# Kernel tuning notes

Hardware: AMD Instinct MI355X
Metric: run time of the kernel (lower is better)

Reference implementation:

```python
import jax, jax.numpy as jnp
import numpy as np

B, N, C, H, W = 4, 5, 64, 96, 288
DOWNSAMPLE_RATE = 4
DISCRETE_RATIO = 0.4
DECAY_WEIGHTS = jax.nn.softmax(jnp.array([1.0, 0.5], dtype=jnp.float32))  # frame=1, decay=0.5


def _warp_one(img, theta):
    # img: (C,H,W), theta: (2,3). Matches F.affine_grid + F.grid_sample
    # (bilinear, zeros padding, align_corners=True).
    c, h, w = img.shape
    xs = jnp.linspace(-1.0, 1.0, w, dtype=img.dtype)
    ys = jnp.linspace(-1.0, 1.0, h, dtype=img.dtype)
    gy, gx = jnp.meshgrid(ys, xs, indexing='ij')
    base = jnp.stack([gx.ravel(), gy.ravel(), jnp.ones(h * w, img.dtype)], 0)  # (3, HW)
    g = theta @ base  # (2, HW) normalized coords
    px = (g[0] + 1.0) * 0.5 * (w - 1)
    py = (g[1] + 1.0) * 0.5 * (h - 1)
    x0 = jnp.floor(px); y0 = jnp.floor(py)
    wx = px - x0; wy = py - y0
    def tap(yy, xx):
        yi = jnp.clip(yy, 0, h - 1).astype(jnp.int32)
        xi = jnp.clip(xx, 0, w - 1).astype(jnp.int32)
        valid = ((yy >= 0) & (yy <= h - 1) & (xx >= 0) & (xx <= w - 1)).astype(img.dtype)
        return img[:, yi, xi] * valid  # (C, HW)
    out = (tap(y0, x0) * (1 - wx) * (1 - wy)
           + tap(y0, x0 + 1) * wx * (1 - wy)
           + tap(y0 + 1, x0) * (1 - wx) * wy
           + tap(y0 + 1, x0 + 1) * wx * wy)
    return out.reshape(c, h, w)


def _frame_score(hist, mlp_w, mlp_b):
    # hist: (B,N,C,H,W) -> per-pixel ego-vs-neighbor attention score (B,N,1,H,W).
    b, n, c, h, w = hist.shape
    node = hist.reshape(b, n, c, h * w).transpose(0, 3, 1, 2)  # (B, P, N, C)
    ego = node[:, :, 0]          # (B, P, C)
    neigh = node[:, :, 1:]       # (B, P, N-1, C)
    # Query rows are all the repeated ego vector -> one row suffices (identical math).
    s = jnp.einsum('bpc,bpkc->bpk', ego, neigh) / jnp.sqrt(jnp.asarray(c, hist.dtype))
    attn = jax.nn.softmax(s, axis=-1)
    ctx = jnp.einsum('bpk,bpkc->bpc', attn, neigh)
    sc = jax.nn.sigmoid(ctx @ mlp_w.T + mlp_b)                   # (B, P, 1)
    sc = jnp.broadcast_to(sc[:, :, None, :], (b, h * w, n - 1, 1))
    ego_sc = jnp.ones((b, h * w, 1, 1), hist.dtype)
    overall = jnp.concatenate([ego_sc, sc], axis=2)              # (B, P, N, 1)
    return overall.transpose(0, 2, 3, 1).reshape(b, n, 1, h, w)


def _forward(x0, x1, pairwise_t_matrix, mlp_w, mlp_b):
    x0g = x0.reshape(B, N, C, H, W)
    x1g = x1.reshape(B, N, C, H, W)

    # --- TemporalSampling: weighted per-frame scores, threshold, 3x3 max-pool ---
    conf = DECAY_WEIGHTS[0] * _frame_score(x0g, mlp_w, mlp_b) \
         + DECAY_WEIGHTS[1] * _frame_score(x1g, mlp_w, mlp_b)      # (B,N,1,H,W)
    mask = jnp.where(conf > 0.5, jnp.float32(1.0), jnp.float32(0.0))
    mask = jax.lax.reduce_window(mask, -jnp.inf, jax.lax.max,
                                 (1, 1, 1, 3, 3), (1, 1, 1, 1, 1), 'SAME')
    x = x0g * mask  # broadcast over C

    # --- normalize pairwise transform to 2x3 affine matrices ---
    t = pairwise_t_matrix[:, :, :, jnp.array([0, 1])][:, :, :, :, jnp.array([0, 1, 3])]  # (B,L,L,2,3)
    t = t.at[..., 0, 1].mul(H / W)
    t = t.at[..., 1, 0].mul(W / H)
    t = t.at[..., 0, 2].set(t[..., 0, 2] / (DOWNSAMPLE_RATE * DISCRETE_RATIO * W) * 2)
    t = t.at[..., 1, 2].set(t[..., 1, 2] / (DOWNSAMPLE_RATE * DISCRETE_RATIO * H) * 2)
    theta = t[:, 0]  # (B,N,2,3): warp each cav into ego frame

    # --- per-agent warp ---
    warped = jax.vmap(jax.vmap(_warp_one))(x, theta)  # (B,N,C,H,W)

    # --- AttenFusion: per-pixel NxN attention, keep ego row ---
    nf = warped.reshape(B, N, C, H * W).transpose(0, 3, 1, 2)  # (B, P, N, C)
    s = jnp.einsum('bpc,bpkc->bpk', nf[:, :, 0], nf) / jnp.sqrt(jnp.asarray(C, nf.dtype))
    attn = jax.nn.softmax(s, axis=-1)
    ctx = jnp.einsum('bpk,bpkc->bpc', attn, nf)                 # (B, P, C)
    x_fuse = ctx.transpose(0, 2, 1).reshape(B, C, H, W)
    return x_fuse


def setup_inputs() -> dict:
    key = jax.random.key(0)
    k0, k1, k2, k3 = jax.random.split(key, 4)
    x0 = jax.random.normal(k0, (B * N, C, H, W), dtype=jnp.float32)
    x1 = jax.random.normal(k1, (B * N, C, H, W), dtype=jnp.float32)
    eye = jnp.broadcast_to(jnp.eye(4, dtype=jnp.float32), (B, N, N, 4, 4))
    pairwise_t_matrix = eye + 0.01 * jax.random.normal(k2, (B, N, N, 4, 4), dtype=jnp.float32)
    mlp_w = 0.1 * jax.random.normal(k3, (1, C), dtype=jnp.float32)
    mlp_b = jnp.zeros((1,), dtype=jnp.float32)
    record_len = jnp.full((B,), N, dtype=jnp.int32)
    return {"x0": x0, "x1": x1, "pairwise_t_matrix": pairwise_t_matrix,
            "mlp_w": mlp_w, "mlp_b": mlp_b, "record_len": record_len}


def reference(x0, x1, pairwise_t_matrix, mlp_w, mlp_b, record_len):
    # record_len is uniform (=N) and only determines the static regrouping.
    return _forward(x0, x1, pairwise_t_matrix, mlp_w, mlp_b)
```

## Files before the change

### kernel.cpp

```cpp
#include <hip/hip_runtime.h>
#include <cmath>

#define BB 4
#define NN 5
#define CC 64
#define HH 96
#define WW 288
#define PP (HH*WW)

static __device__ __forceinline__ float sigmoidf_(float x) {
    return 1.0f / (1.0f + expf(-x));
}

__global__ __launch_bounds__(256) void mask_kernel(
    const float* __restrict__ x0, const float* __restrict__ x1,
    const float* __restrict__ mlp_w, const float* __restrict__ mlp_b,
    float* __restrict__ premask)
{
    int idx = blockIdx.x * blockDim.x + threadIdx.x;
    if (idx >= BB * PP) return;
    int b = idx / PP;
    int p = idx - b * PP;
    float bias = mlp_b[0];

    float scv[2];
    const float* bases[2];
    bases[0] = x0 + (size_t)b * NN * CC * PP + p;
    bases[1] = x1 + (size_t)b * NN * CC * PP + p;

    #pragma unroll
    for (int t = 0; t < 2; t++) {
        const float* base = bases[t];
        float dot0 = 0.f, dot1 = 0.f, dot2 = 0.f, dot3 = 0.f;
        float mw0 = 0.f, mw1 = 0.f, mw2 = 0.f, mw3 = 0.f;
        for (int c = 0; c < CC; c++) {
            const float* q = base + (size_t)c * PP;
            float e  = q[0];
            float wc = mlp_w[c];
            float v1 = q[(size_t)1 * CC * PP];
            float v2 = q[(size_t)2 * CC * PP];
            float v3 = q[(size_t)3 * CC * PP];
            float v4 = q[(size_t)4 * CC * PP];
            dot0 += e * v1;  mw0 += wc * v1;
            dot1 += e * v2;  mw1 += wc * v2;
            dot2 += e * v3;  mw2 += wc * v3;
            dot3 += e * v4;  mw3 += wc * v4;
        }
        float s0 = dot0 * 0.125f, s1 = dot1 * 0.125f;
        float s2 = dot2 * 0.125f, s3 = dot3 * 0.125f;
        float m = fmaxf(fmaxf(s0, s1), fmaxf(s2, s3));
        float e0 = expf(s0 - m), e1 = expf(s1 - m);
        float e2 = expf(s2 - m), e3 = expf(s3 - m);
        float inv = 1.0f / (e0 + e1 + e2 + e3);
        float z = (e0 * mw0 + e1 * mw1 + e2 * mw2 + e3 * mw3) * inv + bias;
        scv[t] = sigmoidf_(z);
    }
    const float W0 = 0.6224593312018546f, W1 = 0.3775406687981454f;
    float conf = W0 * scv[0] + W1 * scv[1];
    premask[idx] = (conf > 0.5f) ? 1.0f : 0.0f;
}

__global__ __launch_bounds__(256) void pool_kernel(
    const float* __restrict__ pre, float* __restrict__ pooled)
{
    int idx = blockIdx.x * blockDim.x + threadIdx.x;
    if (idx >= BB * PP) return;
    int b = idx / PP;
    int p = idx - b * PP;
    int h = p / WW;
    int w = p - h * WW;
    const float* pb = pre + (size_t)b * PP;
    float m = 0.0f;
    #pragma unroll
    for (int dy = -1; dy <= 1; dy++) {
        int y = h + dy;
        if (y < 0 || y >= HH) continue;
        #pragma unroll
        for (int dx = -1; dx <= 1; dx++) {
            int x = w + dx;
            if (x < 0 || x >= WW) continue;
            m = fmaxf(m, pb[y * WW + x]);
        }
    }
    pooled[idx] = m;
}

__global__ __launch_bounds__(256) void fuse_kernel(
    const float* __restrict__ x0, const float* __restrict__ pmat,
    const float* __restrict__ pooled, float* __restrict__ out)
{
    int idx = blockIdx.x * blockDim.x + threadIdx.x;
    if (idx >= BB * PP) return;
    int b = idx / PP;
    int p = idx - b * PP;
    int h = p / WW;
    int w = p - h * WW;

    float gx = -1.0f + 2.0f * (float)w / (float)(WW - 1);
    float gy = -1.0f + 2.0f * (float)h / (float)(HH - 1);

    int   offs[NN][4];
    float wts[NN][4];

    #pragma unroll
    for (int n = 0; n < NN; n++) {
        const float* m = pmat + ((size_t)(b * NN + 0) * NN + n) * 16;
        float t00 = m[0];
        float t01 = m[1] * ((float)HH / (float)WW);
        float t02 = m[3] * (float)(2.0 / (4.0 * 0.4 * (double)WW));
        float t10 = m[4] * ((float)WW / (float)HH);
        float t11 = m[5];
        float t12 = m[7] * (float)(2.0 / (4.0 * 0.4 * (double)HH));

        float g0 = t00 * gx + t01 * gy + t02;
        float g1 = t10 * gx + t11 * gy + t12;
        float px = (g0 + 1.0f) * 0.5f * (float)(WW - 1);
        float py = (g1 + 1.0f) * 0.5f * (float)(HH - 1);
        float x0f = floorf(px), y0f = floorf(py);
        float wx = px - x0f, wy = py - y0f;

        float bw[4] = { (1.f - wx) * (1.f - wy), wx * (1.f - wy),
                        (1.f - wx) * wy,         wx * wy };
        #pragma unroll
        for (int t = 0; t < 4; t++) {
            float xx = (t & 1) ? (x0f + 1.0f) : x0f;
            float yy = (t >> 1) ? (y0f + 1.0f) : y0f;
            int xi = min(max((int)xx, 0), WW - 1);
            int yi = min(max((int)yy, 0), HH - 1);
            float valid = (yy >= 0.0f && yy <= (float)(HH - 1) &&
                           xx >= 0.0f && xx <= (float)(WW - 1)) ? 1.0f : 0.0f;
            float mk = (n == 0) ? 1.0f : pooled[b * PP + yi * WW + xi];
            offs[n][t] = yi * WW + xi;
            wts[n][t]  = bw[t] * valid * mk;
        }
    }

    const float* base = x0 + (size_t)b * NN * CC * PP;

    float dot[NN] = {0.f, 0.f, 0.f, 0.f, 0.f};
    for (int c = 0; c < CC; c++) {
        float v[NN];
        #pragma unroll
        for (int n = 0; n < NN; n++) {
            const float* pl = base + ((size_t)n * CC + c) * PP;
            float acc = 0.f;
            #pragma unroll
            for (int t = 0; t < 4; t++)
                acc += wts[n][t] * pl[offs[n][t]];
            v[n] = acc;
        }
        #pragma unroll
        for (int n = 0; n < NN; n++)
            dot[n] += v[0] * v[n];
    }

    float s[NN], attn[NN];
    float mx = -INFINITY;
    #pragma unroll
    for (int n = 0; n < NN; n++) { s[n] = dot[n] * 0.125f; mx = fmaxf(mx, s[n]); }
    float sum = 0.f;
    #pragma unroll
    for (int n = 0; n < NN; n++) { attn[n] = expf(s[n] - mx); sum += attn[n]; }
    float inv = 1.0f / sum;
    #pragma unroll
    for (int n = 0; n < NN; n++) attn[n] *= inv;

    for (int c = 0; c < CC; c++) {
        float o = 0.f;
        #pragma unroll
        for (int n = 0; n < NN; n++) {
            const float* pl = base + ((size_t)n * CC + c) * PP;
            float acc = 0.f;
            #pragma unroll
            for (int t = 0; t < 4; t++)
                acc += wts[n][t] * pl[offs[n][t]];
            o += attn[n] * acc;
        }
        out[((size_t)b * CC + c) * PP + p] = o;
    }
}

extern "C" void kernel_launch(void* const* d_in, const int* in_sizes, int n_in,
                              void* d_out, int out_size, void* d_ws, size_t ws_size,
                              hipStream_t stream) {
    const float* x0    = (const float*)d_in[0];
    const float* x1    = (const float*)d_in[1];
    const float* pmat  = (const float*)d_in[2];
    const float* mlp_w = (const float*)d_in[3];
    const float* mlp_b = (const float*)d_in[4];
    float* out = (float*)d_out;

    const size_t need = (size_t)2 * BB * PP * sizeof(float);
    float* pre;
    float* pooled;
    if (ws_size >= need && d_ws != nullptr) {
        pre    = (float*)d_ws;
        pooled = pre + (size_t)BB * PP;
    } else {
        pre    = out;
        pooled = (float*)d_in[1];
    }

    int total = BB * PP;
    dim3 blk(256);
    dim3 grd((total + 255) / 256);

    mask_kernel<<<grd, blk, 0, stream>>>(x0, x1, mlp_w, mlp_b, pre);
    pool_kernel<<<grd, blk, 0, stream>>>(pre, pooled);
    fuse_kernel<<<grd, blk, 0, stream>>>(x0, pmat, pooled, out);
}
```

Measured before the change: 407.4 us.

## Split channel loops across grid dimension with partial-sum kernels

```diff
diff --git a/kernel.cpp b/kernel.cpp
--- a/kernel.cpp
+++ b/kernel.cpp
@@ -7,101 +7,21 @@
 #define HH 96
 #define WW 288
 #define PP (HH*WW)
+#define BP (BB*PP)
+#define CP (CC*PP)
+#define NCP (NN*CC*PP)
+
 
 static __device__ __forceinline__ float sigmoidf_(float x) {
     return 1.0f / (1.0f + expf(-x));
 }
 
-__global__ __launch_bounds__(256) void mask_kernel(
-    const float* __restrict__ x0, const float* __restrict__ x1,
-    const float* __restrict__ mlp_w, const float* __restrict__ mlp_b,
-    float* __restrict__ premask)
-{
-    int idx = blockIdx.x * blockDim.x + threadIdx.x;
-    if (idx >= BB * PP) return;
-    int b = idx / PP;
-    int p = idx - b * PP;
-    float bias = mlp_b[0];
-
-    float scv[2];
-    const float* bases[2];
-    bases[0] = x0 + (size_t)b * NN * CC * PP + p;
-    bases[1] = x1 + (size_t)b * NN * CC * PP + p;
-
-    #pragma unroll
-    for (int t = 0; t < 2; t++) {
-        const float* base = bases[t];
-        float dot0 = 0.f, dot1 = 0.f, dot2 = 0.f, dot3 = 0.f;
-        float mw0 = 0.f, mw1 = 0.f, mw2 = 0.f, mw3 = 0.f;
-        for (int c = 0; c < CC; c++) {
-            const float* q = base + (size_t)c * PP;
-            float e  = q[0];
-            float wc = mlp_w[c];
-            float v1 = q[(size_t)1 * CC * PP];
-            float v2 = q[(size_t)2 * CC * PP];
-            float v3 = q[(size_t)3 * CC * PP];
-            float v4 = q[(size_t)4 * CC * PP];
-            dot0 += e * v1;  mw0 += wc * v1;
-            dot1 += e * v2;  mw1 += wc * v2;
-            dot2 += e * v3;  mw2 += wc * v3;
-            dot3 += e * v4;  mw3 += wc * v4;
-        }
-        float s0 = dot0 * 0.125f, s1 = dot1 * 0.125f;
-        float s2 = dot2 * 0.125f, s3 = dot3 * 0.125f;
-        float m = fmaxf(fmaxf(s0, s1), fmaxf(s2, s3));
-        float e0 = expf(s0 - m), e1 = expf(s1 - m);
-        float e2 = expf(s2 - m), e3 = expf(s3 - m);
-        float inv = 1.0f / (e0 + e1 + e2 + e3);
-        float z = (e0 * mw0 + e1 * mw1 + e2 * mw2 + e3 * mw3) * inv + bias;
-        scv[t] = sigmoidf_(z);
-    }
-    const float W0 = 0.6224593312018546f, W1 = 0.3775406687981454f;
-    float conf = W0 * scv[0] + W1 * scv[1];
-    premask[idx] = (conf > 0.5f) ? 1.0f : 0.0f;
-}
-
-__global__ __launch_bounds__(256) void pool_kernel(
-    const float* __restrict__ pre, float* __restrict__ pooled)
-{
-    int idx = blockIdx.x * blockDim.x + threadIdx.x;
-    if (idx >= BB * PP) return;
-    int b = idx / PP;
-    int p = idx - b * PP;
-    int h = p / WW;
-    int w = p - h * WW;
-    const float* pb = pre + (size_t)b * PP;
-    float m = 0.0f;
-    #pragma unroll
-    for (int dy = -1; dy <= 1; dy++) {
-        int y = h + dy;
-        if (y < 0 || y >= HH) continue;
-        #pragma unroll
-        for (int dx = -1; dx <= 1; dx++) {
-            int x = w + dx;
-            if (x < 0 || x >= WW) continue;
-            m = fmaxf(m, pb[y * WW + x]);
-        }
-    }
-    pooled[idx] = m;
-}
-
-__global__ __launch_bounds__(256) void fuse_kernel(
-    const float* __restrict__ x0, const float* __restrict__ pmat,
-    const float* __restrict__ pooled, float* __restrict__ out)
-{
-    int idx = blockIdx.x * blockDim.x + threadIdx.x;
-    if (idx >= BB * PP) return;
-    int b = idx / PP;
-    int p = idx - b * PP;
-    int h = p / WW;
-    int w = p - h * WW;
-
+static __device__ __forceinline__ void tap_setup(
+    int b, int h, int w, const float* __restrict__ pmat,
+    const float* __restrict__ pooled, int offs[NN][4], float wts[NN][4])
+{
     float gx = -1.0f + 2.0f * (float)w / (float)(WW - 1);
     float gy = -1.0f + 2.0f * (float)h / (float)(HH - 1);
-
-    int   offs[NN][4];
-    float wts[NN][4];
-
     #pragma unroll
     for (int n = 0; n < NN; n++) {
         const float* m = pmat + ((size_t)(b * NN + 0) * NN + n) * 16;
@@ -118,7 +38,6 @@
         float py = (g1 + 1.0f) * 0.5f * (float)(HH - 1);
         float x0f = floorf(px), y0f = floorf(py);
         float wx = px - x0f, wy = py - y0f;
-
         float bw[4] = { (1.f - wx) * (1.f - wy), wx * (1.f - wy),
                         (1.f - wx) * wy,         wx * wy };
         #pragma unroll
@@ -134,11 +53,118 @@
             wts[n][t]  = bw[t] * valid * mk;
         }
     }
-
-    const float* base = x0 + (size_t)b * NN * CC * PP;
-
-    float dot[NN] = {0.f, 0.f, 0.f, 0.f, 0.f};
-    for (int c = 0; c < CC; c++) {
+}
+
+__global__ __launch_bounds__(256) void mask_part_kernel(
+    const float* __restrict__ x0, const float* __restrict__ x1,
+    const float* __restrict__ mlp_w, float* __restrict__ mpart)
+{
+    int idx = blockIdx.x * blockDim.x + threadIdx.x;
+    int seg = blockIdx.y;
+    int b = idx / PP;
+    int p = idx - b * PP;
+    const float* xt = (seg >> 2) ? x1 : x0;
+    int c0 = (seg & 3) * 16;
+    const float* base = xt + (size_t)b * NCP + p;
+
+    float d0=0.f,d1=0.f,d2=0.f,d3=0.f, m0=0.f,m1=0.f,m2=0.f,m3=0.f;
+    #pragma unroll 4
+    for (int ci = 0; ci < 16; ci++) {
+        int c = c0 + ci;
+        const float* q = base + (size_t)c * PP;
+        float e  = q[0];
+        float wc = mlp_w[c];
+        float v1 = q[(size_t)1 * CP];
+        float v2 = q[(size_t)2 * CP];
+        float v3 = q[(size_t)3 * CP];
+        float v4 = q[(size_t)4 * CP];
+        d0 += e * v1;  m0 += wc * v1;
+        d1 += e * v2;  m1 += wc * v2;
+        d2 += e * v3;  m2 += wc * v3;
+        d3 += e * v4;  m3 += wc * v4;
+    }
+    float vals[8] = {d0,d1,d2,d3,m0,m1,m2,m3};
+    #pragma unroll
+    for (int j = 0; j < 8; j++)
+        mpart[((size_t)seg * 8 + j) * BP + idx] = vals[j];
+}
+
+__global__ __launch_bounds__(256) void mask_comb_kernel(
+    const float* __restrict__ mpart, const float* __restrict__ mlp_b,
+    float* __restrict__ premask)
+{
+    int idx = blockIdx.x * blockDim.x + threadIdx.x;
+    float bias = mlp_b[0];
+    float scv[2];
+    #pragma unroll
+    for (int t = 0; t < 2; t++) {
+        float d[4] = {0.f,0.f,0.f,0.f};
+        float m[4] = {0.f,0.f,0.f,0.f};
+        #pragma unroll
+        for (int cs = 0; cs < 4; cs++) {
+            int seg = t * 4 + cs;
+            #pragma unroll
+            for (int j = 0; j < 4; j++) {
+                d[j] += mpart[((size_t)seg * 8 + j) * BP + idx];
+                m[j] += mpart[((size_t)seg * 8 + 4 + j) * BP + idx];
+            }
+        }
+        float s0 = d[0]*0.125f, s1 = d[1]*0.125f, s2 = d[2]*0.125f, s3 = d[3]*0.125f;
+        float mx = fmaxf(fmaxf(s0, s1), fmaxf(s2, s3));
+        float e0 = expf(s0-mx), e1 = expf(s1-mx), e2 = expf(s2-mx), e3 = expf(s3-mx);
+        float inv = 1.0f / (e0+e1+e2+e3);
+        float z = (e0*m[0] + e1*m[1] + e2*m[2] + e3*m[3]) * inv + bias;
+        scv[t] = sigmoidf_(z);
+    }
+    const float W0 = 0.6224593312018546f, W1 = 0.3775406687981454f;
+    float conf = W0 * scv[0] + W1 * scv[1];
+    premask[idx] = (conf > 0.5f) ? 1.0f : 0.0f;
+}
+
+__global__ __launch_bounds__(256) void pool_kernel(
+    const float* __restrict__ pre, float* __restrict__ pooled)
+{
+    int idx = blockIdx.x * blockDim.x + threadIdx.x;
+    int b = idx / PP;
+    int p = idx - b * PP;
+    int h = p / WW;
+    int w = p - h * WW;
+    const float* pb = pre + (size_t)b * PP;
+    float m = 0.0f;
+    #pragma unroll
+    for (int dy = -1; dy <= 1; dy++) {
+        int y = h + dy;
+        if (y < 0 || y >= HH) continue;
+        #pragma unroll
+        for (int dx = -1; dx <= 1; dx++) {
+            int x = w + dx;
+            if (x < 0 || x >= WW) continue;
+            m = fmaxf(m, pb[y * WW + x]);
+        }
+    }
+    pooled[idx] = m;
+}
+
+__global__ __launch_bounds__(256) void dot_part_kernel(
+    const float* __restrict__ x0, const float* __restrict__ pmat,
+    const float* __restrict__ pooled, float* __restrict__ dpart)
+{
+    int idx = blockIdx.x * blockDim.x + threadIdx.x;
+    int seg = blockIdx.y;
+    int b = idx / PP;
+    int p = idx - b * PP;
+    int h = p / WW;
+    int w = p - h * WW;
+
+    int offs[NN][4];
+    float wts[NN][4];
+    tap_setup(b, h, w, pmat, pooled, offs, wts);
+
+    const float* base = x0 + (size_t)b * NCP;
+    float dot[NN] = {0.f,0.f,0.f,0.f,0.f};
+    #pragma unroll 4
+    for (int ci = 0; ci < 16; ci++) {
+        int c = seg * 16 + ci;
         float v[NN];
         #pragma unroll
         for (int n = 0; n < NN; n++) {
@@ -153,7 +179,31 @@
         for (int n = 0; n < NN; n++)
             dot[n] += v[0] * v[n];
     }
-
+    #pragma unroll
+    for (int n = 0; n < NN; n++)
+        dpart[((size_t)n * 4 + seg) * BP + idx] = dot[n];
+}
+
+__global__ __launch_bounds__(256) void attn_kernel(
+    const float* __restrict__ dpart, const float* __restrict__ pmat,
+    const float* __restrict__ pooled, float* __restrict__ aw,
+    int* __restrict__ offout)
+{
+    int idx = blockIdx.x * blockDim.x + threadIdx.x;
+    int b = idx / PP;
+    int p = idx - b * PP;
+    int h = p / WW;
+    int w = p - h * WW;
+
+    float dot[NN];
+    #pragma unroll
+    for (int n = 0; n < NN; n++) {
+        float s = 0.f;
+        #pragma unroll
+        for (int seg = 0; seg < 4; seg++)
+            s += dpart[((size_t)n * 4 + seg) * BP + idx];
+        dot[n] = s;
+    }
     float s[NN], attn[NN];
     float mx = -INFINITY;
     #pragma unroll
@@ -162,50 +212,84 @@
     #pragma unroll
     for (int n = 0; n < NN; n++) { attn[n] = expf(s[n] - mx); sum += attn[n]; }
     float inv = 1.0f / sum;
-    #pragma unroll
-    for (int n = 0; n < NN; n++) attn[n] *= inv;
-
-    for (int c = 0; c < CC; c++) {
-        float o = 0.f;
-        #pragma unroll
-        for (int n = 0; n < NN; n++) {
-            const float* pl = base + ((size_t)n * CC + c) * PP;
-            float acc = 0.f;
-            #pragma unroll
-            for (int t = 0; t < 4; t++)
-                acc += wts[n][t] * pl[offs[n][t]];
-            o += attn[n] * acc;
-        }
-        out[((size_t)b * CC + c) * PP + p] = o;
-    }
+
+    int offs[NN][4];
+    float wts[NN][4];
+    tap_setup(b, h, w, pmat, pooled, offs, wts);
+    #pragma unroll
+    for (int n = 0; n < NN; n++) {
+        float a = attn[n] * inv;
+        #pragma unroll
+        for (int t = 0; t < 4; t++) {
+            aw[((size_t)n * 4 + t) * BP + idx]     = a * wts[n][t];
+            offout[((size_t)n * 4 + t) * BP + idx] = offs[n][t];
+        }
+    }
+}
+
+__global__ __launch_bounds__(256) void out_kernel(
+    const float* __restrict__ x0, const float* __restrict__ aw,
+    const int* __restrict__ offin, float* __restrict__ out)
+{
+    int idx = blockIdx.x * blockDim.x + threadIdx.x;
+    int c0  = blockIdx.y * 4;
+    int b = idx / PP;
+    int p = idx - b * PP;
+
+    float a[20];
+    int   o[20];
+    #pragma unroll
+    for (int j = 0; j < 20; j++) {
+        a[j] = aw[(size_t)j * BP + idx];
+        o[j] = offin[(size_t)j * BP + idx];
+    }
+
+    const float* base = x0 + (size_t)b * NCP + (size_t)c0 * PP;
+    float acc0 = 0.f, acc1 = 0.f, acc2 = 0.f, acc3 = 0.f;
+    #pragma unroll
+    for (int j = 0; j < 20; j++) {
+        int n = j >> 2;
+        const float* pl = base + (size_t)n * CP + o[j];
+        float w = a[j];
+        acc0 += w * pl[0];
+        acc1 += w * pl[(size_t)1 * PP];
+        acc2 += w * pl[(size_t)2 * PP];
+        acc3 += w * pl[(size_t)3 * PP];
+    }
+    size_t ob = ((size_t)b * CC + c0) * PP + p;
+    out[ob]                 = acc0;
+    out[ob + (size_t)1*PP]  = acc1;
+    out[ob + (size_t)2*PP]  = acc2;
+    out[ob + (size_t)3*PP]  = acc3;
 }
 
 extern "C" void kernel_launch(void* const* d_in, const int* in_sizes, int n_in,
                               void* d_out, int out_size, void* d_ws, size_t ws_size,
                               hipStream_t stream) {
     const float* x0    = (const float*)d_in[0];
-    const float* x1    = (const float*)d_in[1];
+    float*       x1    = (float*)d_in[1];
     const float* pmat  = (const float*)d_in[2];
     const float* mlp_w = (const float*)d_in[3];
     const float* mlp_b = (const float*)d_in[4];
     float* out = (float*)d_out;
 
-    const size_t need = (size_t)2 * BB * PP * sizeof(float);
-    float* pre;
-    float* pooled;
-    if (ws_size >= need && d_ws != nullptr) {
-        pre    = (float*)d_ws;
-        pooled = pre + (size_t)BB * PP;
-    } else {
-        pre    = out;
-        pooled = (float*)d_in[1];
-    }
-
-    int total = BB * PP;
+    float* mpart  = out;
+    float* s_pre  = x1;
+    float* s_pool = x1 + (size_t)1  * BP;
+    float* s_dot  = x1 + (size_t)2  * BP;
+    float* s_aw   = x1 + (size_t)22 * BP;
+    int*   s_off  = (int*)(x1 + (size_t)42 * BP);
+
     dim3 blk(256);
-    dim3 grd((total + 255) / 256);
-
-    mask_kernel<<<grd, blk, 0, stream>>>(x0, x1, mlp_w, mlp_b, pre);
-    pool_kernel<<<grd, blk, 0, stream>>>(pre, pooled);
-    fuse_kernel<<<grd, blk, 0, stream>>>(x0, pmat, pooled, out);
-}
+    dim3 g1(BP / 256, 8);
+    dim3 g2(BP / 256);
+    dim3 gf1(BP / 256, 4);
+    dim3 gf2(BP / 256, 16);
+
+    mask_part_kernel<<<g1,  blk, 0, stream>>>(x0, x1, mlp_w, mpart);
+    mask_comb_kernel<<<g2,  blk, 0, stream>>>(mpart, mlp_b, s_pre);
+    pool_kernel     <<<g2,  blk, 0, stream>>>(s_pre, s_pool);
+    dot_part_kernel <<<gf1, blk, 0, stream>>>(x0, pmat, s_pool, s_dot);
+    attn_kernel     <<<g2,  blk, 0, stream>>>(s_dot, pmat, s_pool, s_aw, s_off);
+    out_kernel      <<<gf2, blk, 0, stream>>>(x0, s_aw, s_off, out);
+}
```

Result: slower. 474.4 us (+16.4%).
